# Performance work log

Hardware: AMD Instinct MI355X
Metric: run time of the kernel (lower is better)

## Reference

```python
import jax, jax.numpy as jnp
import numpy as np

KERNEL_NUM = 21
SIGMA = 0.1
EXACT_SIGMA = 0.001

def _kernel_params():
    mus, sigmas = [], []
    for i in range(KERNEL_NUM):
        mu = 1.0 / (KERNEL_NUM - 1) + 2.0 * i / (KERNEL_NUM - 1) - 1.0
        sigma = SIGMA
        if mu > 1.0:
            sigma = EXACT_SIGMA
            mu = 1.0
        mus.append(mu)
        sigmas.append(sigma)
    return np.asarray(mus, np.float32), np.asarray(sigmas, np.float32)

MU, SIG = _kernel_params()  # [K], [K]

def setup_inputs() -> dict:
    key = jax.random.key(0)
    k = jax.random.split(key, 8)
    V, D, B, L, R = 50000, 128, 512, 30, 200
    emb = jax.random.normal(k[0], (V, D), dtype=jnp.float32)
    W = jax.random.normal(k[1], (1, KERNEL_NUM), dtype=jnp.float32) * 0.1
    b = jax.random.normal(k[2], (1,), dtype=jnp.float32) * 0.1
    query1 = jax.random.randint(k[3], (B, L), 0, V, dtype=jnp.int32)
    doc1 = jax.random.randint(k[4], (B, R), 0, V, dtype=jnp.int32)
    query2 = jax.random.randint(k[5], (B, L), 0, V, dtype=jnp.int32)
    doc2 = jax.random.randint(k[6], (B, R), 0, V, dtype=jnp.int32)
    return {"emb": emb, "W": W, "b": b, "query1": query1, "doc1": doc1,
            "query2": query2, "doc2": doc2}

def _l2norm(x):
    # F.normalize(p=2, dim=-1): x / max(||x||, eps)
    n = jnp.sqrt(jnp.sum(x * x, axis=-1, keepdims=True))
    return x / jnp.maximum(n, 1e-12)

def _predict(emb, W, b, q, d):
    eq = _l2norm(emb[q])              # [B,L,D]
    ed = _l2norm(emb[d])              # [B,R,D]
    M = jnp.einsum('bld,brd->blr', eq, ed)  # matching matrix [B,L,R]
    # multi-Gaussian kernel bank: [B,L,R,K]
    Kmat = jnp.exp(-0.5 * (M[..., None] - MU) ** 2 / (SIG ** 2))
    km = jnp.sum(jnp.log1p(jnp.sum(Kmat, axis=2)), axis=1)  # [B,K]
    return km @ W.T + b               # [B,1]

def reference(emb, W, b, query1, doc1, query2, doc2):
    logits1 = _predict(emb, W, b, query1, doc1)
    logits2 = _predict(emb, W, b, query2, doc2)
    return jax.nn.sigmoid(logits1 - logits2)
```

## Files before the change

kernel.cpp:

```cpp
#include <hip/hip_runtime.h>
#include <hip/hip_fp16.h>
#include <math.h>

#define V   50000
#define DIM 128
#define BB  512
#define LQ  30
#define RD  200
#define KN  21

typedef __attribute__((ext_vector_type(8))) _Float16 f16x8;
typedef __attribute__((ext_vector_type(4))) float f32x4;
typedef __attribute__((ext_vector_type(2))) float f32x2;

#if __has_builtin(__builtin_amdgcn_exp2f)
#define EXP2F(x) __builtin_amdgcn_exp2f(x)
#else
#define EXP2F(x) __expf((x) * 0.69314718f)
#endif

#define ALPHA 72.1347520f
#define E10   22026.4657948f

static __device__ __forceinline__ f16x8 as_hfrag(int4 v) {
    return __builtin_bit_cast(f16x8, v);
}
static __device__ __forceinline__ unsigned pk2h(float a, float b) {
    return __builtin_bit_cast(unsigned, __builtin_amdgcn_cvt_pkrtz(a, b));
}
static __device__ __forceinline__ unsigned hscale(unsigned u, __half2 s) {
    return __builtin_bit_cast(unsigned, __hmul2(__builtin_bit_cast(__half2, u), s));
}

static __device__ __forceinline__ void gather_row_f16(const float* __restrict__ rowp,
                                                      int g, int4* f) {
    float ss = 0.0f;
#pragma unroll
    for (int ks = 0; ks < 4; ++ks) {
        const float4* p = reinterpret_cast<const float4*>(rowp + ks * 32 + g * 8);
        float4 a = p[0], b = p[1];
        ss = fmaf(a.x, a.x, fmaf(a.y, a.y, fmaf(a.z, a.z, fmaf(a.w, a.w, ss))));
        ss = fmaf(b.x, b.x, fmaf(b.y, b.y, fmaf(b.z, b.z, fmaf(b.w, b.w, ss))));
        f[ks].x = (int)pk2h(a.x, a.y);
        f[ks].y = (int)pk2h(a.z, a.w);
        f[ks].z = (int)pk2h(b.x, b.y);
        f[ks].w = (int)pk2h(b.z, b.w);
    }
    ss += __shfl_xor(ss, 16);
    ss += __shfl_xor(ss, 32);
    const float inv = rsqrtf(fmaxf(ss, 1e-24f));
    const __half2 h2 = __float2half2_rn(inv);
#pragma unroll
    for (int ks = 0; ks < 4; ++ks) {
        f[ks].x = (int)hscale((unsigned)f[ks].x, h2);
        f[ks].y = (int)hscale((unsigned)f[ks].y, h2);
        f[ks].z = (int)hscale((unsigned)f[ks].z, h2);
        f[ks].w = (int)hscale((unsigned)f[ks].w, h2);
    }
}

static __device__ __forceinline__ void bank4_pk(f32x4 pv, int4 dt, int qt,
                                                f32x2* ks2, float& cnt) {
    const float mv[4] = {pv[0], pv[1], pv[2], pv[3]};
    const int   dv[4] = {dt.x, dt.y, dt.z, dt.w};
    f32x2 t[4], u[4];
#pragma unroll
    for (int i = 0; i < 4; ++i) {
        float m  = mv[i];
        float dA = m + 0.5f, dB = m - 0.5f;
        float tA = EXP2F(-ALPHA * dA * (dA + 0.9f));
        float tB = EXP2F(-ALPHA * dB * (dB + 0.9f));
        float uB = EXP2F(14.4269504f * dB);
        float uA = uB * E10;
        t[i] = f32x2{tA, tB};
        u[i] = f32x2{uA, uB};
        cnt += (dv[i] == qt) ? 1.0f : 0.0f;
    }
#pragma unroll
    for (int k = 0; k < 10; ++k) {
        ks2[k] += (t[0] + t[1]) + (t[2] + t[3]);
        t[0] *= u[0]; t[1] *= u[1]; t[2] *= u[2]; t[3] *= u[3];
    }
}

__global__ __launch_bounds__(256, 4) void knrm_main(
    const float* __restrict__ emb, const float* __restrict__ W,
    const int* __restrict__ q1, const int* __restrict__ d1,
    const int* __restrict__ q2, const int* __restrict__ d2,
    float* __restrict__ logits)
{
    __shared__ int sQtok[32];
    __shared__ __align__(16) int sDtok[256];
    __shared__ int4 sQ[32][16];
    __shared__ float kred[4][32][KN];

    const int pb = blockIdx.x;
    const int pair = pb >> 9, b = pb & 511;
    const int* qind = (pair ? q2 : q1) + b * LQ;
    const int* dind = (pair ? d2 : d1) + b * RD;

    const int tid = threadIdx.x;
    const int lane = tid & 63, w = tid >> 6;
    const int r = lane & 15, g = lane >> 4;

    if (tid < 32) sQtok[tid] = (tid < LQ) ? qind[tid] : -2;
    sDtok[tid] = dind[tid < RD ? tid : RD - 1];

    {
        const int row = tid >> 3, seg = tid & 7;
        const int qi = qind[row < LQ ? row : LQ - 1];
        const float4* p = reinterpret_cast<const float4*>(emb + (size_t)qi * DIM + seg * 16);
        float4 v0 = p[0], v1 = p[1], v2 = p[2], v3 = p[3];
        float ss = 0.0f;
        ss = fmaf(v0.x, v0.x, fmaf(v0.y, v0.y, fmaf(v0.z, v0.z, fmaf(v0.w, v0.w, ss))));
        ss = fmaf(v1.x, v1.x, fmaf(v1.y, v1.y, fmaf(v1.z, v1.z, fmaf(v1.w, v1.w, ss))));
        ss = fmaf(v2.x, v2.x, fmaf(v2.y, v2.y, fmaf(v2.z, v2.z, fmaf(v2.w, v2.w, ss))));
        ss = fmaf(v3.x, v3.x, fmaf(v3.y, v3.y, fmaf(v3.z, v3.z, fmaf(v3.w, v3.w, ss))));
        ss += __shfl_xor(ss, 1);
        ss += __shfl_xor(ss, 2);
        ss += __shfl_xor(ss, 4);
        const float inv = rsqrtf(fmaxf(ss, 1e-24f));
        int4 s0, s1;
        s0.x = (int)pk2h(v0.x * inv, v0.y * inv);
        s0.y = (int)pk2h(v0.z * inv, v0.w * inv);
        s0.z = (int)pk2h(v1.x * inv, v1.y * inv);
        s0.w = (int)pk2h(v1.z * inv, v1.w * inv);
        s1.x = (int)pk2h(v2.x * inv, v2.y * inv);
        s1.y = (int)pk2h(v2.z * inv, v2.w * inv);
        s1.z = (int)pk2h(v3.x * inv, v3.y * inv);
        s1.w = (int)pk2h(v3.z * inv, v3.w * inv);
        const int rw = row & 15;
        sQ[row][(2 * seg) ^ rw]     = s0;
        sQ[row][(2 * seg + 1) ^ rw] = s1;
    }
    __syncthreads();

    int4 qa[4], qb[4];
#pragma unroll
    for (int ks = 0; ks < 4; ++ks) {
        qa[ks] = sQ[r][(ks * 4 + g) ^ r];
        qb[ks] = sQ[16 + r][(ks * 4 + g) ^ r];
    }
    const int qt0 = sQtok[r], qt1 = sQtok[16 + r];
    const int4* sDtok4 = (const int4*)sDtok;

    f32x2 ks0[10], ks1[10];
#pragma unroll
    for (int k = 0; k < 10; ++k) { ks0[k] = f32x2{0.f, 0.f}; ks1[k] = f32x2{0.f, 0.f}; }
    float cnt0 = 0.0f, cnt1 = 0.0f;

    auto strip = [&](int sbase) {
        const int di = sDtok[sbase + r];
        int4 df[4];
        gather_row_f16(emb + (size_t)di * DIM, g, df);
        f32x4 acc0 = {0.f, 0.f, 0.f, 0.f}, acc1 = {0.f, 0.f, 0.f, 0.f};
#pragma unroll
        for (int ks = 0; ks < 4; ++ks) {
            f16x8 fd = as_hfrag(df[ks]);
            acc0 = __builtin_amdgcn_mfma_f32_16x16x32_f16(fd, as_hfrag(qa[ks]), acc0, 0, 0, 0);
            acc1 = __builtin_amdgcn_mfma_f32_16x16x32_f16(fd, as_hfrag(qb[ks]), acc1, 0, 0, 0);
        }
        if (sbase + g * 4 < RD) {
            const int4 dt = sDtok4[(sbase >> 2) + g];
            bank4_pk(acc0, dt, qt0, ks0, cnt0);
            bank4_pk(acc1, dt, qt1, ks1, cnt1);
        }
    };

    if (w < 3) {
#pragma unroll 2
        for (int s = 0; s < 4; ++s) strip(w * 64 + s * 16);
    } else {
        strip(192);
    }

#pragma unroll
    for (int k = 0; k < 10; ++k) {
        float a0 = ks0[k].x, b0 = ks0[k].y, a1 = ks1[k].x, b1 = ks1[k].y;
        a0 += __shfl_xor(a0, 16); a0 += __shfl_xor(a0, 32);
        b0 += __shfl_xor(b0, 16); b0 += __shfl_xor(b0, 32);
        a1 += __shfl_xor(a1, 16); a1 += __shfl_xor(a1, 32);
        b1 += __shfl_xor(b1, 16); b1 += __shfl_xor(b1, 32);
        ks0[k] = f32x2{a0, b0};
        ks1[k] = f32x2{a1, b1};
    }
    cnt0 += __shfl_xor(cnt0, 16); cnt0 += __shfl_xor(cnt0, 32);
    cnt1 += __shfl_xor(cnt1, 16); cnt1 += __shfl_xor(cnt1, 32);

    if (lane < 16) {
        float* k0 = &kred[w][r][0];
        float* k1 = &kred[w][16 + r][0];
#pragma unroll
        for (int k = 0; k < 10; ++k) {
            k0[k] = ks0[k].x;  k0[10 + k] = ks0[k].y;
            k1[k] = ks1[k].x;  k1[10 + k] = ks1[k].y;
        }
        k0[20] = cnt0;
        k1[20] = cnt1;
    }
    __syncthreads();

    if (tid < 64) {
        float part = 0.0f;
        if (tid < LQ) {
#pragma unroll
            for (int k = 0; k < KN; ++k) {
                float s = kred[0][tid][k] + kred[1][tid][k]
                        + kred[2][tid][k] + kred[3][tid][k];
                float sc = 1.0f;
                if (k < 20) {
                    float j = (float)((k < 10) ? k : k - 10) - 4.5f;
                    sc = EXP2F(-0.721347520f * j * j);
                }
                part += W[k] * log1pf(sc * s);
            }
        }
        part += __shfl_xor(part, 1);
        part += __shfl_xor(part, 2);
        part += __shfl_xor(part, 4);
        part += __shfl_xor(part, 8);
        part += __shfl_xor(part, 16);
        part += __shfl_xor(part, 32);
        if (tid == 0) logits[pair * BB + b] = part;
    }
}

__global__ void knrm_final(const float* __restrict__ logits, float* __restrict__ out) {
    int i = blockIdx.x * blockDim.x + threadIdx.x;
    if (i < BB) {
        float x = logits[i] - logits[BB + i];
        out[i] = 1.0f / (1.0f + expf(-x));
    }
}

extern "C" void kernel_launch(void* const* d_in, const int* in_sizes, int n_in,
                              void* d_out, int out_size, void* d_ws, size_t ws_size,
                              hipStream_t stream) {
    const float* emb = (const float*)d_in[0];
    const float* W   = (const float*)d_in[1];
    const int* q1    = (const int*)d_in[3];
    const int* dd1   = (const int*)d_in[4];
    const int* q2    = (const int*)d_in[5];
    const int* dd2   = (const int*)d_in[6];

    float* logits = (float*)d_ws;

    knrm_main<<<1024, 256, 0, stream>>>(emb, W, q1, dd1, q2, dd2, logits);
    knrm_final<<<2, 256, 0, stream>>>(logits, (float*)d_out);
}
```

Before: 33.98 us.

## Split document dimension across two blocks and move log1p reduction to finish kernel

Each (pair,batch) block is split into two blocks along the document axis, giving a 2048-block grid. Each block writes per-query kernel sums to workspace, and a new finish kernel sums the two halves, applies log1p, weights by W and computes the sigmoid. Query normalization now scales in fp16 after packing, and the sum-of-squares chains are split into independent accumulators for more ILP. The split raises parallelism and shortens per-block latency, at the cost of gathering query embeddings twice and extra global traffic for the partial sums.

```diff
diff --git a/kernel.cpp b/kernel.cpp
--- a/kernel.cpp
+++ b/kernel.cpp
@@ -34,18 +34,19 @@
 
 static __device__ __forceinline__ void gather_row_f16(const float* __restrict__ rowp,
                                                       int g, int4* f) {
-    float ss = 0.0f;
+    float c0 = 0.f, c1 = 0.f, c2 = 0.f, c3 = 0.f;
 #pragma unroll
     for (int ks = 0; ks < 4; ++ks) {
         const float4* p = reinterpret_cast<const float4*>(rowp + ks * 32 + g * 8);
         float4 a = p[0], b = p[1];
-        ss = fmaf(a.x, a.x, fmaf(a.y, a.y, fmaf(a.z, a.z, fmaf(a.w, a.w, ss))));
-        ss = fmaf(b.x, b.x, fmaf(b.y, b.y, fmaf(b.z, b.z, fmaf(b.w, b.w, ss))));
+        c0 = fmaf(a.x, a.x, fmaf(a.y, a.y, c0)); c1 = fmaf(a.z, a.z, fmaf(a.w, a.w, c1));
+        c2 = fmaf(b.x, b.x, fmaf(b.y, b.y, c2)); c3 = fmaf(b.z, b.z, fmaf(b.w, b.w, c3));
         f[ks].x = (int)pk2h(a.x, a.y);
         f[ks].y = (int)pk2h(a.z, a.w);
         f[ks].z = (int)pk2h(b.x, b.y);
         f[ks].w = (int)pk2h(b.z, b.w);
     }
+    float ss = (c0 + c1) + (c2 + c3);
     ss += __shfl_xor(ss, 16);
     ss += __shfl_xor(ss, 32);
     const float inv = rsqrtf(fmaxf(ss, 1e-24f));
@@ -84,17 +85,17 @@
 }
 
 __global__ __launch_bounds__(256, 4) void knrm_main(
-    const float* __restrict__ emb, const float* __restrict__ W,
+    const float* __restrict__ emb,
     const int* __restrict__ q1, const int* __restrict__ d1,
     const int* __restrict__ q2, const int* __restrict__ d2,
-    float* __restrict__ logits)
+    float* __restrict__ partial)
 {
     __shared__ int sQtok[32];
     __shared__ __align__(16) int sDtok[256];
     __shared__ int4 sQ[32][16];
     __shared__ float kred[4][32][KN];
 
-    const int pb = blockIdx.x;
+    const int pb = blockIdx.x, y = blockIdx.y;
     const int pair = pb >> 9, b = pb & 511;
     const int* qind = (pair ? q2 : q1) + b * LQ;
     const int* dind = (pair ? d2 : d1) + b * RD;
@@ -111,27 +112,29 @@
         const int qi = qind[row < LQ ? row : LQ - 1];
         const float4* p = reinterpret_cast<const float4*>(emb + (size_t)qi * DIM + seg * 16);
         float4 v0 = p[0], v1 = p[1], v2 = p[2], v3 = p[3];
-        float ss = 0.0f;
-        ss = fmaf(v0.x, v0.x, fmaf(v0.y, v0.y, fmaf(v0.z, v0.z, fmaf(v0.w, v0.w, ss))));
-        ss = fmaf(v1.x, v1.x, fmaf(v1.y, v1.y, fmaf(v1.z, v1.z, fmaf(v1.w, v1.w, ss))));
-        ss = fmaf(v2.x, v2.x, fmaf(v2.y, v2.y, fmaf(v2.z, v2.z, fmaf(v2.w, v2.w, ss))));
-        ss = fmaf(v3.x, v3.x, fmaf(v3.y, v3.y, fmaf(v3.z, v3.z, fmaf(v3.w, v3.w, ss))));
+        float s0 = 0.f, s1 = 0.f, s2 = 0.f, s3 = 0.f;
+        s0 = fmaf(v0.x, v0.x, fmaf(v0.y, v0.y, s0)); s1 = fmaf(v0.z, v0.z, fmaf(v0.w, v0.w, s1));
+        s2 = fmaf(v1.x, v1.x, fmaf(v1.y, v1.y, s2)); s3 = fmaf(v1.z, v1.z, fmaf(v1.w, v1.w, s3));
+        s0 = fmaf(v2.x, v2.x, fmaf(v2.y, v2.y, s0)); s1 = fmaf(v2.z, v2.z, fmaf(v2.w, v2.w, s1));
+        s2 = fmaf(v3.x, v3.x, fmaf(v3.y, v3.y, s2)); s3 = fmaf(v3.z, v3.z, fmaf(v3.w, v3.w, s3));
+        float ss = (s0 + s1) + (s2 + s3);
         ss += __shfl_xor(ss, 1);
         ss += __shfl_xor(ss, 2);
         ss += __shfl_xor(ss, 4);
         const float inv = rsqrtf(fmaxf(ss, 1e-24f));
-        int4 s0, s1;
-        s0.x = (int)pk2h(v0.x * inv, v0.y * inv);
-        s0.y = (int)pk2h(v0.z * inv, v0.w * inv);
-        s0.z = (int)pk2h(v1.x * inv, v1.y * inv);
-        s0.w = (int)pk2h(v1.z * inv, v1.w * inv);
-        s1.x = (int)pk2h(v2.x * inv, v2.y * inv);
-        s1.y = (int)pk2h(v2.z * inv, v2.w * inv);
-        s1.z = (int)pk2h(v3.x * inv, v3.y * inv);
-        s1.w = (int)pk2h(v3.z * inv, v3.w * inv);
+        const __half2 h2 = __float2half2_rn(inv);
+        int4 t0, t1;
+        t0.x = (int)hscale(pk2h(v0.x, v0.y), h2);
+        t0.y = (int)hscale(pk2h(v0.z, v0.w), h2);
+        t0.z = (int)hscale(pk2h(v1.x, v1.y), h2);
+        t0.w = (int)hscale(pk2h(v1.z, v1.w), h2);
+        t1.x = (int)hscale(pk2h(v2.x, v2.y), h2);
+        t1.y = (int)hscale(pk2h(v2.z, v2.w), h2);
+        t1.z = (int)hscale(pk2h(v3.x, v3.y), h2);
+        t1.w = (int)hscale(pk2h(v3.z, v3.w), h2);
         const int rw = row & 15;
-        sQ[row][(2 * seg) ^ rw]     = s0;
-        sQ[row][(2 * seg + 1) ^ rw] = s1;
+        sQ[row][(2 * seg) ^ rw]     = t0;
+        sQ[row][(2 * seg + 1) ^ rw] = t1;
     }
     __syncthreads();
 
@@ -167,11 +170,12 @@
         }
     };
 
-    if (w < 3) {
-#pragma unroll 2
-        for (int s = 0; s < 4; ++s) strip(w * 64 + s * 16);
+    if (y == 0) {
+        if (w < 3) { strip(w * 32); strip(w * 32 + 16); }
+        else       { strip(96); }
     } else {
-        strip(192);
+        if (w < 2) { strip(112 + w * 32); strip(128 + w * 32); }
+        else       { strip(176 + (w - 2) * 16); }
     }
 
 #pragma unroll
@@ -200,36 +204,41 @@
     }
     __syncthreads();
 
-    if (tid < 64) {
-        float part = 0.0f;
-        if (tid < LQ) {
-#pragma unroll
-            for (int k = 0; k < KN; ++k) {
-                float s = kred[0][tid][k] + kred[1][tid][k]
-                        + kred[2][tid][k] + kred[3][tid][k];
-                float sc = 1.0f;
-                if (k < 20) {
-                    float j = (float)((k < 10) ? k : k - 10) - 4.5f;
-                    sc = EXP2F(-0.721347520f * j * j);
-                }
-                part += W[k] * log1pf(sc * s);
-            }
-        }
-        part += __shfl_xor(part, 1);
-        part += __shfl_xor(part, 2);
-        part += __shfl_xor(part, 4);
-        part += __shfl_xor(part, 8);
-        part += __shfl_xor(part, 16);
-        part += __shfl_xor(part, 32);
-        if (tid == 0) logits[pair * BB + b] = part;
-    }
-}
-
-__global__ void knrm_final(const float* __restrict__ logits, float* __restrict__ out) {
-    int i = blockIdx.x * blockDim.x + threadIdx.x;
-    if (i < BB) {
-        float x = logits[i] - logits[BB + i];
-        out[i] = 1.0f / (1.0f + expf(-x));
+    float* dst = partial + ((size_t)pb * 2 + y) * (LQ * KN);
+    for (int e = tid; e < LQ * KN; e += 256) {
+        int row = e / KN, k = e - row * KN;
+        float s = kred[0][row][k] + kred[1][row][k]
+                + kred[2][row][k] + kred[3][row][k];
+        float sc = 1.0f;
+        if (k < 20) {
+            float j = (float)((k < 10) ? k : k - 10) - 4.5f;
+            sc = EXP2F(-0.721347520f * j * j);
+        }
+        dst[e] = sc * s;
+    }
+}
+
+__global__ __launch_bounds__(128) void knrm_finish(const float* __restrict__ partial,
+                                                   const float* __restrict__ W,
+                                                   float* __restrict__ out) {
+    __shared__ float red[2];
+    const int b = blockIdx.x, tid = threadIdx.x;
+    const float* p1 = partial + (size_t)(b * 2) * (LQ * KN);
+    const float* p2 = partial + (size_t)((BB + b) * 2) * (LQ * KN);
+    float s = 0.0f;
+    for (int e = tid; e < LQ * KN; e += 128) {
+        int row = e / KN, k = e - row * KN;
+        float s1 = p1[e] + p1[LQ * KN + e];
+        float s2 = p2[e] + p2[LQ * KN + e];
+        s += W[k] * (log1pf(s1) - log1pf(s2));
+    }
+#pragma unroll
+    for (int off = 1; off < 64; off <<= 1) s += __shfl_xor(s, off);
+    if ((tid & 63) == 0) red[tid >> 6] = s;
+    __syncthreads();
+    if (tid == 0) {
+        float logit = red[0] + red[1];
+        out[b] = 1.0f / (1.0f + expf(-logit));
     }
 }
 
@@ -243,8 +252,9 @@
     const int* q2    = (const int*)d_in[5];
     const int* dd2   = (const int*)d_in[6];
 
-    float* logits = (float*)d_ws;
-
-    knrm_main<<<1024, 256, 0, stream>>>(emb, W, q1, dd1, q2, dd2, logits);
-    knrm_final<<<2, 256, 0, stream>>>(logits, (float*)d_out);
-}
+    float* partial = (float*)d_ws;
+
+    dim3 grid(1024, 2);
+    knrm_main<<<grid, 256, 0, stream>>>(emb, q1, dd1, q2, dd2, partial);
+    knrm_finish<<<BB, 128, 0, stream>>>(partial, W, (float*)d_out);
+}
```

Result: slower. 38.82 us (+14.2%).
